# Kernel optimization log

Hardware: AMD Instinct MI355X
Metric: run time of the kernel (lower is better)

Reference implementation:

```python
import jax, jax.numpy as jnp
import numpy as np

N = 50000   # nodes
E = 400000  # edges per relation
R = 3       # relations
IN, HID, OUT, H = 256, 64, 64, 4
NEG_SLOPE = 0.2


def setup_inputs() -> dict:
    key = jax.random.key(0)
    ks = jax.random.split(key, 16)
    w = lambda k, shape, s: jax.random.normal(k, shape, jnp.float32) * s
    sW = 1.0 / np.sqrt(IN)  # ~xavier scale (all fan-ins are 256)
    return {
        "x":   w(ks[0], (N, IN), 1.0),
        "src": jax.random.randint(ks[1], (R, E), 0, N, jnp.int32),
        "dst": jax.random.randint(ks[2], (R, E), 0, N, jnp.int32),
        "W0":  w(ks[3], (R, IN, H * HID), sW),
        "al0": w(ks[4], (R, H, HID), 0.1),
        "ar0": w(ks[5], (R, H, HID), 0.1),
        "b0":  jnp.zeros((R, H * HID), jnp.float32),
        "W1":  w(ks[6], (R, H * HID, H * HID), sW),
        "al1": w(ks[7], (R, H, HID), 0.1),
        "ar1": w(ks[8], (R, H, HID), 0.1),
        "b1":  jnp.zeros((R, H * HID), jnp.float32),
        "W2":  w(ks[9], (R, H * HID, H * OUT), sW),
        "al2": w(ks[10], (R, H, OUT), 0.1),
        "ar2": w(ks[11], (R, H, OUT), 0.1),
        "b2":  jnp.zeros((R, H * OUT), jnp.float32),
    }


def gat_conv(h, src, dst, W, al, ar, b):
    """One DGL-style GATConv with elu activation. h: (N, F_in)."""
    heads, d = al.shape
    feat = (h @ W).reshape(-1, heads, d)               # (N, H, D)
    el = jnp.einsum('nhd,hd->nh', feat, al)            # (N, H)
    er = jnp.einsum('nhd,hd->nh', feat, ar)
    e = jax.nn.leaky_relu(el[src] + er[dst], NEG_SLOPE)  # (E, H)
    # segment softmax over incoming edges of each dst node
    emax = jax.ops.segment_max(e, dst, num_segments=N)
    ex = jnp.exp(e - emax[dst])
    denom = jax.ops.segment_sum(ex, dst, num_segments=N)
    alpha = ex / jnp.maximum(denom[dst], 1e-9)         # (E, H)
    msg = feat[src] * alpha[:, :, None]                # (E, H, D)
    out = jax.ops.segment_sum(msg, dst, num_segments=N)  # (N, H, D)
    out = out + b.reshape(heads, d)
    return jax.nn.elu(out)


def _rgat(x, src, dst, params):
    h = x
    for li, (W, al, ar, b) in enumerate(params):
        outs = [gat_conv(h, src[r], dst[r], W[r], al[r], ar[r], b[r]) for r in range(R)]
        o = sum(outs) / R                              # cross-relation mean, (N, H, D)
        h = o.mean(1) if li == 2 else o.reshape(N, -1)
    return h


def reference(x, src, dst, W0, al0, ar0, b0, W1, al1, ar1, b1, W2, al2, ar2, b2):
    params = [(W0, al0, ar0, b0), (W1, al1, ar1, b1), (W2, al2, ar2, b2)]
    return _rgat(x, src, dst, params)
```

## Files before the change

kernel.cpp:

```cpp
#include <hip/hip_runtime.h>
#include <hip/hip_bf16.h>

#define N_NODES 50000
#define N_EDGES 400000
#define N_REL   3
#define NEG_SLOPE 0.2f
#define RP_STRIDE 50016
#define SCAN_BLOCKS 49
#define M_TILES 391
#define MG_PER_XCD 49
#define M_PAD 50048
#define MAXDEG 48

typedef __bf16 bf16x8 __attribute__((ext_vector_type(8)));
typedef float  f32x4  __attribute__((ext_vector_type(4)));

static __device__ __forceinline__ float bf2f(unsigned short u) {
  return __uint_as_float(((unsigned)u) << 16);
}
static __device__ __forceinline__ unsigned short f2bf(float f) {
  union { float f; unsigned u; } x; x.f = f;
  unsigned r = x.u + 0x7FFFu + ((x.u >> 16) & 1u);
  return (unsigned short)(r >> 16);
}
static __device__ __forceinline__ void gld16(const void* g, unsigned short* lds) {
  __builtin_amdgcn_global_load_lds(
      (const __attribute__((address_space(1))) unsigned int*)g,
      (__attribute__((address_space(3))) unsigned int*)lds, 16, 0, 0);
}


__global__ void count_kernel(const int* __restrict__ dst, int* __restrict__ cnt, int total) {
  int i = blockIdx.x * 256 + threadIdx.x;
  if (i < total) {
    int r = i / N_EDGES;
    atomicAdd(&cnt[r * N_NODES + dst[i]], 1);
  }
}

__global__ void block_reduce_kernel(const int* __restrict__ cnt, int* __restrict__ psum) {
  __shared__ int s[256];
  int r = blockIdx.x / SCAN_BLOCKS, b = blockIdx.x % SCAN_BLOCKS;
  int node = b * 1024 + threadIdx.x * 4;
  int sum = 0;
  if (node + 3 < N_NODES) {
    int4 v = *(const int4*)&cnt[r * N_NODES + node];
    sum = v.x + v.y + v.z + v.w;
  } else {
    for (int j = 0; j < 4; j++)
      if (node + j < N_NODES) sum += cnt[r * N_NODES + node + j];
  }
  s[threadIdx.x] = sum;
  __syncthreads();
  for (int o = 128; o > 0; o >>= 1) {
    if (threadIdx.x < o) s[threadIdx.x] += s[threadIdx.x + o];
    __syncthreads();
  }
  if (threadIdx.x == 0) psum[r * SCAN_BLOCKS + b] = s[0];
}

__global__ void psum_scan_kernel(int* __restrict__ psum, int* __restrict__ row_ptr) {
  int r = blockIdx.x, t = threadIdx.x;
  int v = (t < SCAN_BLOCKS) ? psum[r * SCAN_BLOCKS + t] : 0;
  int incl = v;
#pragma unroll
  for (int o = 1; o < 64; o <<= 1) {
    int u = __shfl_up(incl, o);
    if (t >= o) incl += u;
  }
  if (t < SCAN_BLOCKS) psum[r * SCAN_BLOCKS + t] = incl - v;
  if (t == SCAN_BLOCKS - 1) row_ptr[r * RP_STRIDE + N_NODES] = incl;
}

__global__ void scan_write_kernel(const int* __restrict__ cnt, const int* __restrict__ psum,
                                  int* __restrict__ row_ptr, int* __restrict__ cursor) {
  __shared__ int s[256];
  int r = blockIdx.x / SCAN_BLOCKS, b = blockIdx.x % SCAN_BLOCKS;
  int tid = threadIdx.x;
  int node = b * 1024 + tid * 4;
  int c[4] = {0, 0, 0, 0};
  if (node + 3 < N_NODES) {
    int4 v = *(const int4*)&cnt[r * N_NODES + node];
    c[0] = v.x; c[1] = v.y; c[2] = v.z; c[3] = v.w;
  } else {
    for (int j = 0; j < 4; j++)
      if (node + j < N_NODES) c[j] = cnt[r * N_NODES + node + j];
  }
  int tsum = c[0] + c[1] + c[2] + c[3];
  s[tid] = tsum;
  __syncthreads();
  for (int o = 1; o < 256; o <<= 1) {
    int v = (tid >= o) ? s[tid - o] : 0;
    __syncthreads();
    s[tid] += v;
    __syncthreads();
  }
  int run = s[tid] - tsum + psum[r * SCAN_BLOCKS + b];
  if (node + 3 < N_NODES) {
    int4 rp = make_int4(run, run + c[0], run + c[0] + c[1], run + c[0] + c[1] + c[2]);
    *(int4*)&row_ptr[r * RP_STRIDE + node] = rp;
    *(int4*)&cursor[r * N_NODES + node] = rp;
  } else {
    for (int j = 0; j < 4; j++) {
      if (node + j < N_NODES) {
        row_ptr[r * RP_STRIDE + node + j] = run;
        cursor[r * N_NODES + node + j] = run;
      }
      run += c[j];
    }
  }
}

__global__ void scatter_kernel(const int* __restrict__ src, const int* __restrict__ dst,
                               int* __restrict__ cursor, int* __restrict__ col, int total) {
  int i = blockIdx.x * 256 + threadIdx.x;
  if (i < total) {
    int r = i / N_EDGES;
    int d = dst[i];
    int pos = atomicAdd(&cursor[r * N_NODES + d], 1);
    col[r * N_EDGES + pos] = src[i];
  }
}


__global__ void xsplit_kernel(const float* __restrict__ x, unsigned short* __restrict__ xh) {
  int i = blockIdx.x * 256 + threadIdx.x;
  int row = i >> 6;
  float4 v = make_float4(0.f, 0.f, 0.f, 0.f);
  if (row < N_NODES) v = ((const float4*)x)[i];
  ushort4 h;
  h.x = f2bf(v.x); h.y = f2bf(v.y); h.z = f2bf(v.z); h.w = f2bf(v.w);
  ((ushort4*)xh)[i] = h;
}


__global__ void wsplit_kernel(const float* __restrict__ W0, const float* __restrict__ W1,
                              const float* __restrict__ W2,
                              unsigned short* __restrict__ Whi, unsigned short* __restrict__ Wlo) {
  __shared__ float tile[32][33];
  int mat = blockIdx.x >> 6;
  int t = blockIdx.x & 63;
  int k0 = (t >> 3) * 32, n0 = (t & 7) * 32;
  const float* W = (mat < 3 ? W0 : (mat < 6 ? W1 : W2)) + (size_t)(mat % 3) * 65536;
  int row = threadIdx.x >> 3;
  int c4 = threadIdx.x & 7;
  float4 v = *(const float4*)&W[(k0 + row) * 256 + n0 + c4 * 4];
  tile[c4 * 4 + 0][row] = v.x;
  tile[c4 * 4 + 1][row] = v.y;
  tile[c4 * 4 + 2][row] = v.z;
  tile[c4 * 4 + 3][row] = v.w;
  __syncthreads();
  int nl = threadIdx.x >> 3;
  int kq = threadIdx.x & 7;
  ushort4 h, l;
  float a0 = tile[nl][kq * 4 + 0], a1 = tile[nl][kq * 4 + 1];
  float a2 = tile[nl][kq * 4 + 2], a3 = tile[nl][kq * 4 + 3];
  h.x = f2bf(a0); l.x = f2bf(a0 - bf2f(h.x));
  h.y = f2bf(a1); l.y = f2bf(a1 - bf2f(h.y));
  h.z = f2bf(a2); l.z = f2bf(a2 - bf2f(h.z));
  h.w = f2bf(a3); l.w = f2bf(a3 - bf2f(h.w));
  size_t o = (size_t)mat * 65536 + (n0 + nl) * 256 + k0 + kq * 4;
  *(ushort4*)&Whi[o] = h;
  *(ushort4*)&Wlo[o] = l;
}


#define LDS_S 32
#define LDT  136
#define PLANE 4096
#define BUFSZ (3 * PLANE)

__global__ __launch_bounds__(256, 3) void gemm_mfma_kernel(
    const unsigned short* __restrict__ Ah,
    const unsigned short* __restrict__ Bhi, const unsigned short* __restrict__ Blo,
    const float* __restrict__ alf, const float* __restrict__ arf,
    unsigned short* __restrict__ Cb, float* __restrict__ el, float* __restrict__ er, int M) {
  __shared__ __align__(16) unsigned short lds[2 * BUFSZ];

  const int wid = blockIdx.x;
  const int xcd = wid & 7, local = wid >> 3;
  const int m_t = (local / 6) * 8 + xcd;
  if (m_t >= M_TILES) return;
  const int n_t = local % 6;
  const int m0 = m_t * 128, n0 = n_t * 128;

  const int tid = threadIdx.x;
  const int wave = tid >> 6, lane = tid & 63;
  const int quad = lane >> 4, l16 = lane & 15;
  const int wr = wave & 1, wc = wave >> 1;

  f32x4 acc[4][4];
#pragma unroll
  for (int i = 0; i < 4; i++)
#pragma unroll
    for (int j = 0; j < 4; j++) acc[i][j] = (f32x4){0.f, 0.f, 0.f, 0.f};

  auto stage = [&](int kb, int b) {
    unsigned short* As = lds + b * BUFSZ;
#pragma unroll
    for (int i = 0; i < 2; i++) {
      int ch = wave * 2 + i;
      int c = ch * 64 + lane;
      int row = c >> 2, k16 = c & 3;
      int k16s = k16 ^ ((row >> 1) & 3);
      size_t gA = ((size_t)(m0 + row) * 256 + kb * 32) * 2 + (size_t)k16s * 16;
      size_t gB = ((size_t)(n0 + row) * 256 + kb * 32) * 2 + (size_t)k16s * 16;
      gld16((const char*)Ah + gA, &As[ch * 512]);
      gld16((const char*)Bhi + gB, &As[PLANE + ch * 512]);
      gld16((const char*)Blo + gB, &As[2 * PLANE + ch * 512]);
    }
  };

  stage(0, 0);
  __syncthreads();
  for (int kb = 0; kb < 8; kb++) {
    const int b = kb & 1;
    if (kb < 7) stage(kb + 1, b ^ 1);

    const unsigned short* As = lds + b * BUFSZ;
    const unsigned short* Bh = As + PLANE;
    const unsigned short* Bl = As + 2 * PLANE;
    bf16x8 ah[4], bh[4], bl[4];
#pragma unroll
    for (int t = 0; t < 4; t++) {
      int ar = wr * 64 + t * 16 + l16;
      int br = wc * 64 + t * 16 + l16;
      int ac = quad ^ ((ar >> 1) & 3);
      int bc = quad ^ ((br >> 1) & 3);
      ah[t] = *(const bf16x8*)&As[ar * LDS_S + ac * 8];
      bh[t] = *(const bf16x8*)&Bh[br * LDS_S + bc * 8];
      bl[t] = *(const bf16x8*)&Bl[br * LDS_S + bc * 8];
    }
#pragma unroll
    for (int mi = 0; mi < 4; mi++)
#pragma unroll
      for (int ni = 0; ni < 4; ni++) {
        acc[mi][ni] = __builtin_amdgcn_mfma_f32_16x16x32_bf16(ah[mi], bl[ni], acc[mi][ni], 0, 0, 0);
        acc[mi][ni] = __builtin_amdgcn_mfma_f32_16x16x32_bf16(ah[mi], bh[ni], acc[mi][ni], 0, 0, 0);
      }
    __syncthreads();
  }

  const int hw = n_t * 2 + wc;
  const int rel = hw >> 2, hh = hw & 3;
  float alw[4], arw[4];
#pragma unroll
  for (int ni = 0; ni < 4; ni++) {
    int gc = n0 + wc * 64 + ni * 16 + l16;
    alw[ni] = alf[gc]; arw[ni] = arf[gc];
  }
  float pel[4][4], per_[4][4];
#pragma unroll
  for (int mi = 0; mi < 4; mi++)
#pragma unroll
    for (int r = 0; r < 4; r++) {
      float se = 0.f, sr = 0.f;
#pragma unroll
      for (int ni = 0; ni < 4; ni++) {
        se += acc[mi][ni][r] * alw[ni];
        sr += acc[mi][ni][r] * arw[ni];
      }
      pel[mi][r] = se; per_[mi][r] = sr;
    }
#pragma unroll
  for (int off = 1; off < 16; off <<= 1)
#pragma unroll
    for (int mi = 0; mi < 4; mi++)
#pragma unroll
      for (int r = 0; r < 4; r++) {
        pel[mi][r] += __shfl_xor(pel[mi][r], off);
        per_[mi][r] += __shfl_xor(per_[mi][r], off);
      }
  if (l16 == 0) {
#pragma unroll
    for (int mi = 0; mi < 4; mi++)
#pragma unroll
      for (int r = 0; r < 4; r++) {
        int gm = m0 + wr * 64 + mi * 16 + quad * 4 + r;
        if (gm < M) {
          size_t o = ((size_t)rel * N_NODES + gm) * 4 + hh;
          el[o] = pel[mi][r];
          er[o] = per_[mi][r];
        }
      }
  }

#pragma unroll
  for (int mi = 0; mi < 4; mi++) {
    int row = wr * 64 + mi * 16 + quad * 4;
#pragma unroll
    for (int ni = 0; ni < 4; ni++) {
      int c = wc * 64 + ni * 16 + l16;
#pragma unroll
      for (int r = 0; r < 4; r++)
        lds[(row + r) * LDT + c] = f2bf(acc[mi][ni][r]);
    }
  }
  __syncthreads();
#pragma unroll
  for (int it = 0; it < 8; it++) {
    int chunk = tid + 256 * it;
    int row = chunk >> 4, c8 = (chunk & 15) * 8;
    int gm = m0 + row;
    if (gm < M)
      *(uint4*)&Cb[(size_t)gm * 768 + n0 + c8] = *(const uint4*)&lds[row * LDT + c8];
  }
}


__global__ void agg_kernel(const unsigned short* __restrict__ featb,
                           const float* __restrict__ el, const float* __restrict__ er,
                           const int* __restrict__ row_ptr, const int* __restrict__ col,
                           const float* __restrict__ bias,
                           unsigned short* __restrict__ hH, float* __restrict__ outF,
                           int final_layer) {
  __shared__ float salpha[4][N_REL][MAXDEG * 4];
  __shared__ int   sidx[4][N_REL][MAXDEG];
  int w = threadIdx.x >> 6;
  int n = blockIdx.x * 4 + w;
  int L = threadIdx.x & 63;
  if (n >= N_NODES) return;
  const int hsel = L >> 4;
  const int e1 = L >> 2, h1 = L & 3;

  int s0r[N_REL], s1r[N_REL];
  float invsel[N_REL];

  int sv[N_REL];
  bool val[N_REL];
#pragma unroll
  for (int r = 0; r < N_REL; r++) {
    int s0 = row_ptr[r * RP_STRIDE + n], s1 = row_ptr[r * RP_STRIDE + n + 1];
    s0r[r] = s0; s1r[r] = s1;
    int deg = s1 - s0;
    val[r] = (e1 < deg);
    sv[r] = val[r] ? col[(size_t)r * N_EDGES + s0 + e1] : 0;
  }
  float ernh1[N_REL], elv[N_REL];
#pragma unroll
  for (int r = 0; r < N_REL; r++)
    ernh1[r] = er[((size_t)r * N_NODES + n) * 4 + h1];
#pragma unroll
  for (int r = 0; r < N_REL; r++)
    elv[r] = val[r] ? el[((size_t)r * N_NODES + sv[r]) * 4 + h1] : 0.f;
#pragma unroll
  for (int r = 0; r < N_REL; r++) {
    int s0 = s0r[r], deg = s1r[r] - s0r[r];
    float e = elv[r] + ernh1[r];
    e = e > 0.f ? e : NEG_SLOPE * e;
    float p = val[r] ? __expf(e) : 0.f;
    if (val[r] && deg <= MAXDEG) {
      salpha[w][r][e1 * 4 + h1] = p;
      if (h1 == 0) sidx[w][r][e1] = sv[r];
    }
    float d = p;
    for (int base = 16; base < deg; base += 16) {
      int e2 = base + e1;
      bool v2 = e2 < deg;
      int s = v2 ? col[(size_t)r * N_EDGES + s0 + e2] : 0;
      float elx = v2 ? el[((size_t)r * N_NODES + s) * 4 + h1] : 0.f;
      float ee = elx + ernh1[r];
      ee = ee > 0.f ? ee : NEG_SLOPE * ee;
      float pp = v2 ? __expf(ee) : 0.f;
      if (v2 && deg <= MAXDEG) {
        salpha[w][r][e2 * 4 + h1] = pp;
        if (h1 == 0) sidx[w][r][e2] = s;
      }
      d += pp;
    }
#pragma unroll
    for (int o = 4; o < 64; o <<= 1) d += __shfl_xor(d, o);
    float inv = 1.0f / fmaxf(d, 1e-30f);
    invsel[r] = __shfl(inv, hsel);
  }
  __builtin_amdgcn_wave_barrier();

  const float third = 1.0f / 3.0f;
  const int roffL = 4 * L;
  float os0 = 0.f, os1 = 0.f, os2 = 0.f, os3 = 0.f;
#pragma unroll
  for (int r = 0; r < N_REL; r++) {
    int s0 = s0r[r], s1 = s1r[r], deg = s1 - s0;
    const int roff = r * 256 + roffL;
    float a0 = 0.f, a1 = 0.f, a2 = 0.f, a3 = 0.f;
    const float inv = invsel[r];
    float4 bv = *(const float4*)&bias[r * 256 + roffL];
    if (deg <= MAXDEG) {
      const float* ap = &salpha[w][r][0];
      const int* ip = &sidx[w][r][0];
      int i = 0;
      for (; i + 8 <= deg; i += 8) {
        int s_[8];
#pragma unroll
        for (int j = 0; j < 8; j++) s_[j] = ip[i + j];
        ushort4 f_[8];
#pragma unroll
        for (int j = 0; j < 8; j++) {
          size_t ro = (size_t)(unsigned)__builtin_amdgcn_readfirstlane(s_[j]) * 768;
          f_[j] = *(const ushort4*)&featb[ro + roff];
        }
        float w_[8];
#pragma unroll
        for (int j = 0; j < 8; j++) w_[j] = ap[(i + j) * 4 + hsel];
#pragma unroll
        for (int j = 0; j < 8; j++) {
          a0 += w_[j] * bf2f(f_[j].x);
          a1 += w_[j] * bf2f(f_[j].y);
          a2 += w_[j] * bf2f(f_[j].z);
          a3 += w_[j] * bf2f(f_[j].w);
        }
      }
      for (; i + 4 <= deg; i += 4) {
        int s_[4];
#pragma unroll
        for (int j = 0; j < 4; j++) s_[j] = ip[i + j];
        ushort4 f_[4];
#pragma unroll
        for (int j = 0; j < 4; j++) {
          size_t ro = (size_t)(unsigned)__builtin_amdgcn_readfirstlane(s_[j]) * 768;
          f_[j] = *(const ushort4*)&featb[ro + roff];
        }
        float w_[4];
#pragma unroll
        for (int j = 0; j < 4; j++) w_[j] = ap[(i + j) * 4 + hsel];
#pragma unroll
        for (int j = 0; j < 4; j++) {
          a0 += w_[j] * bf2f(f_[j].x);
          a1 += w_[j] * bf2f(f_[j].y);
          a2 += w_[j] * bf2f(f_[j].z);
          a3 += w_[j] * bf2f(f_[j].w);
        }
      }
      for (; i < deg; i++) {
        int sA = ip[i];
        size_t ro = (size_t)(unsigned)__builtin_amdgcn_readfirstlane(sA) * 768;
        ushort4 fA = *(const ushort4*)&featb[ro + roff];
        float wA = ap[i * 4 + hsel];
        a0 += wA * bf2f(fA.x); a1 += wA * bf2f(fA.y);
        a2 += wA * bf2f(fA.z); a3 += wA * bf2f(fA.w);
      }
    } else {
      float ernh2 = er[((size_t)r * N_NODES + n) * 4 + hsel];
      const int* cp = col + (size_t)r * N_EDGES;
      for (int i = s0; i < s1; i++) {
        int s = cp[i];
        float elh = el[((size_t)r * N_NODES + s) * 4 + hsel];
        float e = elh + ernh2; e = e > 0.f ? e : NEG_SLOPE * e;
        float pw = __expf(e);
        ushort4 fA = *(const ushort4*)&featb[(size_t)s * 768 + roff];
        a0 += pw * bf2f(fA.x); a1 += pw * bf2f(fA.y);
        a2 += pw * bf2f(fA.z); a3 += pw * bf2f(fA.w);
      }
    }
    float o0 = a0 * inv + bv.x, o1 = a1 * inv + bv.y;
    float o2 = a2 * inv + bv.z, o3 = a3 * inv + bv.w;
    o0 = o0 > 0.f ? o0 : __expf(o0) - 1.0f;
    o1 = o1 > 0.f ? o1 : __expf(o1) - 1.0f;
    o2 = o2 > 0.f ? o2 : __expf(o2) - 1.0f;
    o3 = o3 > 0.f ? o3 : __expf(o3) - 1.0f;
    os0 += o0 * third; os1 += o1 * third; os2 += o2 * third; os3 += o3 * third;
  }
  if (final_layer) {
#pragma unroll
    for (int o = 16; o <= 32; o <<= 1) {
      os0 += __shfl_xor(os0, o); os1 += __shfl_xor(os1, o);
      os2 += __shfl_xor(os2, o); os3 += __shfl_xor(os3, o);
    }
    if (L < 16)
      *(float4*)&outF[(size_t)n * 64 + L * 4] =
          make_float4(0.25f * os0, 0.25f * os1, 0.25f * os2, 0.25f * os3);
  } else {
    ushort4 h;
    h.x = f2bf(os0); h.y = f2bf(os1); h.z = f2bf(os2); h.w = f2bf(os3);
    *(ushort4*)&hH[(size_t)n * 256 + 4 * L] = h;
  }
}


extern "C" void kernel_launch(void* const* d_in, const int* in_sizes, int n_in,
                              void* d_out, int out_size, void* d_ws, size_t ws_size,
                              hipStream_t stream) {
  (void)in_sizes; (void)n_in; (void)out_size; (void)ws_size;
  const float* x = (const float*)d_in[0];
  const int* src = (const int*)d_in[1];
  const int* dst = (const int*)d_in[2];
  const float* Wl[3]  = {(const float*)d_in[3], (const float*)d_in[7], (const float*)d_in[11]};
  const float* alL[3] = {(const float*)d_in[4], (const float*)d_in[8], (const float*)d_in[12]};
  const float* arL[3] = {(const float*)d_in[5], (const float*)d_in[9], (const float*)d_in[13]};
  const float* bL[3]  = {(const float*)d_in[6], (const float*)d_in[10], (const float*)d_in[14]};

  char* p = (char*)d_ws;
  auto alloc = [&](size_t bytes) {
    char* q = p;
    p += (bytes + 255) & ~size_t(255);
    return q;
  };
  unsigned short* xh = (unsigned short*)alloc((size_t)M_PAD * 256 * 2);
  unsigned short* hH = (unsigned short*)alloc((size_t)M_PAD * 256 * 2);
  unsigned short* featb = (unsigned short*)alloc((size_t)N_NODES * 768 * 2);
  float* el      = (float*)alloc((size_t)N_REL * N_NODES * 4 * 4);
  float* er      = (float*)alloc((size_t)N_REL * N_NODES * 4 * 4);
  int*   cnt     = (int*)alloc((size_t)N_REL * N_NODES * 4);
  int*   cursor  = (int*)alloc((size_t)N_REL * N_NODES * 4);
  int*   row_ptr = (int*)alloc((size_t)N_REL * RP_STRIDE * 4 + 64);
  int*   col     = (int*)alloc((size_t)N_REL * N_EDGES * 4);
  int*   psum    = (int*)alloc((size_t)N_REL * SCAN_BLOCKS * 4);
  unsigned short* Whi = (unsigned short*)alloc((size_t)9 * 65536 * 2);
  unsigned short* Wlo = (unsigned short*)alloc((size_t)9 * 65536 * 2);

  hipMemsetAsync(cnt, 0, (size_t)N_REL * N_NODES * 4, stream);
  const int totalE = N_REL * N_EDGES;
  count_kernel<<<(totalE + 255) / 256, 256, 0, stream>>>(dst, cnt, totalE);
  block_reduce_kernel<<<N_REL * SCAN_BLOCKS, 256, 0, stream>>>(cnt, psum);
  psum_scan_kernel<<<N_REL, 64, 0, stream>>>(psum, row_ptr);
  scan_write_kernel<<<N_REL * SCAN_BLOCKS, 256, 0, stream>>>(cnt, psum, row_ptr, cursor);
  scatter_kernel<<<(totalE + 255) / 256, 256, 0, stream>>>(src, dst, cursor, col, totalE);
  wsplit_kernel<<<9 * 64, 256, 0, stream>>>(Wl[0], Wl[1], Wl[2], Whi, Wlo);
  xsplit_kernel<<<M_PAD * 64 / 256, 256, 0, stream>>>(x, xh);

  const int nodeBlocks = (N_NODES + 3) / 4;
  const int gemmBlocks = MG_PER_XCD * 6 * 8;
  for (int l = 0; l < 3; l++) {
    const unsigned short* Ahp = (l == 0) ? xh : hH;
    gemm_mfma_kernel<<<gemmBlocks, 256, 0, stream>>>(
        Ahp, Whi + (size_t)l * 3 * 65536, Wlo + (size_t)l * 3 * 65536,
        alL[l], arL[l], featb, el, er, N_NODES);
    agg_kernel<<<nodeBlocks, 256, 0, stream>>>(
        featb, el, er, row_ptr, col, bL[l], hH, (float*)d_out, l == 2);
  }
}
```

Before: 736.1 us.

## Keep attention weights in registers and prefetch next relation's gathers

Drops the LDS staging of per-edge softmax weights and source indices in the aggregation kernel. Weights are pre-normalized in registers and broadcast via shuffles, and source indices come from readlane. Feature gathers for the next relation are issued before the current relation is consumed, giving software pipelining across the three relations. Nodes with degree above 16 now take the slow serial fallback (previously above 48), and the live feature buffers raise register pressure.

Result: no change. 740.6 us (+0.6%).

```diff
diff --git a/kernel.cpp b/kernel.cpp
--- a/kernel.cpp
+++ b/kernel.cpp
@@ -10,7 +10,6 @@
 #define M_TILES 391
 #define MG_PER_XCD 49
 #define M_PAD 50048
-#define MAXDEG 48
 
 typedef __bf16 bf16x8 __attribute__((ext_vector_type(8)));
 typedef float  f32x4  __attribute__((ext_vector_type(4)));
@@ -308,25 +307,84 @@
 }
 
 
+#define CONSUME8(F, PN, R, BASE, a0, a1, a2, a3)                         \
+  {                                                                      \
+    _Pragma("unroll")                                                    \
+    for (int j = 0; j < 8; j++) {                                        \
+      float wj = __shfl(PN[R], (BASE + j) * 4 + hsel);                   \
+      a0 += wj * bf2f(F[j].x);                                           \
+      a1 += wj * bf2f(F[j].y);                                           \
+      a2 += wj * bf2f(F[j].z);                                           \
+      a3 += wj * bf2f(F[j].w);                                           \
+    }                                                                    \
+  }
+
+#define ISSUE8(F, R, BASE)                                               \
+  {                                                                      \
+    const unsigned short* fb_ = featb + (R) * 256 + roffL;               \
+    _Pragma("unroll")                                                    \
+    for (int j = 0; j < 8; j++) {                                        \
+      unsigned s_ = (unsigned)__builtin_amdgcn_readlane(sv[R], (BASE + j) * 4); \
+      F[j] = *(const ushort4*)&fb_[(size_t)s_ * 768];                    \
+    }                                                                    \
+  }
+
+#define REL_BODY(R, FCUR, FNXT, NR)                                      \
+  {                                                                      \
+    int deg = s1r[R] - s0r[R];                                           \
+    if ((NR) >= 0) ISSUE8(FNXT, NR, 0);                                  \
+    float a0 = 0.f, a1 = 0.f, a2 = 0.f, a3 = 0.f;                        \
+    float4 bv = *(const float4*)&bias[(R) * 256 + roffL];                \
+    if (deg <= 16) {                                                     \
+      if (deg > 8) {                                                     \
+        ushort4 g[8];                                                    \
+        ISSUE8(g, R, 8);                                                 \
+        CONSUME8(FCUR, pnorm, R, 0, a0, a1, a2, a3);                     \
+        CONSUME8(g, pnorm, R, 8, a0, a1, a2, a3);                        \
+      } else {                                                           \
+        CONSUME8(FCUR, pnorm, R, 0, a0, a1, a2, a3);                     \
+      }                                                                  \
+    } else {                                                             \
+      float ernh2 = er[((size_t)(R) * N_NODES + n) * 4 + hsel];          \
+      const int* cp = col + (size_t)(R) * N_EDGES;                       \
+      const unsigned short* fb_ = featb + (R) * 256 + roffL;             \
+      a0 = a1 = a2 = a3 = 0.f;                                           \
+      for (int i = s0r[R]; i < s1r[R]; i++) {                            \
+        int s_ = cp[i];                                                  \
+        float elh = el[((size_t)(R) * N_NODES + s_) * 4 + hsel];         \
+        float e_ = elh + ernh2; e_ = e_ > 0.f ? e_ : NEG_SLOPE * e_;     \
+        float pw = __expf(e_);                                           \
+        ushort4 fA = *(const ushort4*)&fb_[(size_t)s_ * 768];            \
+        a0 += pw * bf2f(fA.x); a1 += pw * bf2f(fA.y);                    \
+        a2 += pw * bf2f(fA.z); a3 += pw * bf2f(fA.w);                    \
+      }                                                                  \
+      float inv = invsel_[R];                                            \
+      a0 *= inv; a1 *= inv; a2 *= inv; a3 *= inv;                        \
+    }                                                                    \
+    float o0 = a0 + bv.x, o1 = a1 + bv.y, o2 = a2 + bv.z, o3 = a3 + bv.w;\
+    o0 = o0 > 0.f ? o0 : __expf(o0) - 1.0f;                              \
+    o1 = o1 > 0.f ? o1 : __expf(o1) - 1.0f;                              \
+    o2 = o2 > 0.f ? o2 : __expf(o2) - 1.0f;                              \
+    o3 = o3 > 0.f ? o3 : __expf(o3) - 1.0f;                              \
+    os0 += o0 * third; os1 += o1 * third;                                \
+    os2 += o2 * third; os3 += o3 * third;                                \
+  }
+
 __global__ void agg_kernel(const unsigned short* __restrict__ featb,
                            const float* __restrict__ el, const float* __restrict__ er,
                            const int* __restrict__ row_ptr, const int* __restrict__ col,
                            const float* __restrict__ bias,
                            unsigned short* __restrict__ hH, float* __restrict__ outF,
                            int final_layer) {
-  __shared__ float salpha[4][N_REL][MAXDEG * 4];
-  __shared__ int   sidx[4][N_REL][MAXDEG];
   int w = threadIdx.x >> 6;
   int n = blockIdx.x * 4 + w;
   int L = threadIdx.x & 63;
   if (n >= N_NODES) return;
   const int hsel = L >> 4;
   const int e1 = L >> 2, h1 = L & 3;
-
-  int s0r[N_REL], s1r[N_REL];
-  float invsel[N_REL];
-
-  int sv[N_REL];
+  const int roffL = 4 * L;
+
+  int s0r[N_REL], s1r[N_REL], sv[N_REL];
   bool val[N_REL];
 #pragma unroll
   for (int r = 0; r < N_REL; r++) {
@@ -343,123 +401,40 @@
 #pragma unroll
   for (int r = 0; r < N_REL; r++)
     elv[r] = val[r] ? el[((size_t)r * N_NODES + sv[r]) * 4 + h1] : 0.f;
+
+  ushort4 FA[8], FB[8];
+  ISSUE8(FA, 0, 0);
+
+  float pnorm[N_REL], invsel_[N_REL];
 #pragma unroll
   for (int r = 0; r < N_REL; r++) {
-    int s0 = s0r[r], deg = s1r[r] - s0r[r];
+    int deg = s1r[r] - s0r[r];
     float e = elv[r] + ernh1[r];
     e = e > 0.f ? e : NEG_SLOPE * e;
     float p = val[r] ? __expf(e) : 0.f;
-    if (val[r] && deg <= MAXDEG) {
-      salpha[w][r][e1 * 4 + h1] = p;
-      if (h1 == 0) sidx[w][r][e1] = sv[r];
-    }
     float d = p;
     for (int base = 16; base < deg; base += 16) {
       int e2 = base + e1;
       bool v2 = e2 < deg;
-      int s = v2 ? col[(size_t)r * N_EDGES + s0 + e2] : 0;
+      int s = v2 ? col[(size_t)r * N_EDGES + s0r[r] + e2] : 0;
       float elx = v2 ? el[((size_t)r * N_NODES + s) * 4 + h1] : 0.f;
       float ee = elx + ernh1[r];
       ee = ee > 0.f ? ee : NEG_SLOPE * ee;
-      float pp = v2 ? __expf(ee) : 0.f;
-      if (v2 && deg <= MAXDEG) {
-        salpha[w][r][e2 * 4 + h1] = pp;
-        if (h1 == 0) sidx[w][r][e2] = s;
-      }
-      d += pp;
+      d += v2 ? __expf(ee) : 0.f;
     }
 #pragma unroll
     for (int o = 4; o < 64; o <<= 1) d += __shfl_xor(d, o);
-    float inv = 1.0f / fmaxf(d, 1e-30f);
-    invsel[r] = __shfl(inv, hsel);
-  }
-  __builtin_amdgcn_wave_barrier();
+    float rinv = 1.0f / fmaxf(d, 1e-30f);
+    pnorm[r] = p * rinv;
+    invsel_[r] = __shfl(rinv, hsel);
+  }
 
   const float third = 1.0f / 3.0f;
-  const int roffL = 4 * L;
   float os0 = 0.f, os1 = 0.f, os2 = 0.f, os3 = 0.f;
-#pragma unroll
-  for (int r = 0; r < N_REL; r++) {
-    int s0 = s0r[r], s1 = s1r[r], deg = s1 - s0;
-    const int roff = r * 256 + roffL;
-    float a0 = 0.f, a1 = 0.f, a2 = 0.f, a3 = 0.f;
-    const float inv = invsel[r];
-    float4 bv = *(const float4*)&bias[r * 256 + roffL];
-    if (deg <= MAXDEG) {
-      const float* ap = &salpha[w][r][0];
-      const int* ip = &sidx[w][r][0];
-      int i = 0;
-      for (; i + 8 <= deg; i += 8) {
-        int s_[8];
-#pragma unroll
-        for (int j = 0; j < 8; j++) s_[j] = ip[i + j];
-        ushort4 f_[8];
-#pragma unroll
-        for (int j = 0; j < 8; j++) {
-          size_t ro = (size_t)(unsigned)__builtin_amdgcn_readfirstlane(s_[j]) * 768;
-          f_[j] = *(const ushort4*)&featb[ro + roff];
-        }
-        float w_[8];
-#pragma unroll
-        for (int j = 0; j < 8; j++) w_[j] = ap[(i + j) * 4 + hsel];
-#pragma unroll
-        for (int j = 0; j < 8; j++) {
-          a0 += w_[j] * bf2f(f_[j].x);
-          a1 += w_[j] * bf2f(f_[j].y);
-          a2 += w_[j] * bf2f(f_[j].z);
-          a3 += w_[j] * bf2f(f_[j].w);
-        }
-      }
-      for (; i + 4 <= deg; i += 4) {
-        int s_[4];
-#pragma unroll
-        for (int j = 0; j < 4; j++) s_[j] = ip[i + j];
-        ushort4 f_[4];
-#pragma unroll
-        for (int j = 0; j < 4; j++) {
-          size_t ro = (size_t)(unsigned)__builtin_amdgcn_readfirstlane(s_[j]) * 768;
-          f_[j] = *(const ushort4*)&featb[ro + roff];
-        }
-        float w_[4];
-#pragma unroll
-        for (int j = 0; j < 4; j++) w_[j] = ap[(i + j) * 4 + hsel];
-#pragma unroll
-        for (int j = 0; j < 4; j++) {
-          a0 += w_[j] * bf2f(f_[j].x);
-          a1 += w_[j] * bf2f(f_[j].y);
-          a2 += w_[j] * bf2f(f_[j].z);
-          a3 += w_[j] * bf2f(f_[j].w);
-        }
-      }
-      for (; i < deg; i++) {
-        int sA = ip[i];
-        size_t ro = (size_t)(unsigned)__builtin_amdgcn_readfirstlane(sA) * 768;
-        ushort4 fA = *(const ushort4*)&featb[ro + roff];
-        float wA = ap[i * 4 + hsel];
-        a0 += wA * bf2f(fA.x); a1 += wA * bf2f(fA.y);
-        a2 += wA * bf2f(fA.z); a3 += wA * bf2f(fA.w);
-      }
-    } else {
-      float ernh2 = er[((size_t)r * N_NODES + n) * 4 + hsel];
-      const int* cp = col + (size_t)r * N_EDGES;
-      for (int i = s0; i < s1; i++) {
-        int s = cp[i];
-        float elh = el[((size_t)r * N_NODES + s) * 4 + hsel];
-        float e = elh + ernh2; e = e > 0.f ? e : NEG_SLOPE * e;
-        float pw = __expf(e);
-        ushort4 fA = *(const ushort4*)&featb[(size_t)s * 768 + roff];
-        a0 += pw * bf2f(fA.x); a1 += pw * bf2f(fA.y);
-        a2 += pw * bf2f(fA.z); a3 += pw * bf2f(fA.w);
-      }
-    }
-    float o0 = a0 * inv + bv.x, o1 = a1 * inv + bv.y;
-    float o2 = a2 * inv + bv.z, o3 = a3 * inv + bv.w;
-    o0 = o0 > 0.f ? o0 : __expf(o0) - 1.0f;
-    o1 = o1 > 0.f ? o1 : __expf(o1) - 1.0f;
-    o2 = o2 > 0.f ? o2 : __expf(o2) - 1.0f;
-    o3 = o3 > 0.f ? o3 : __expf(o3) - 1.0f;
-    os0 += o0 * third; os1 += o1 * third; os2 += o2 * third; os3 += o3 * third;
-  }
+  REL_BODY(0, FA, FB, 1);
+  REL_BODY(1, FB, FA, 2);
+  REL_BODY(2, FA, FB, -1);
+
   if (final_layer) {
 #pragma unroll
     for (int o = 16; o <= 32; o <<= 1) {
```
